# Kernel optimization log

Measured on AMD Instinct MI355X. Metric: run time of the kernel, lower is better.

The kernel has to match this reference:

```python
import math
import jax, jax.numpy as jnp
import numpy as np

B, S, H, M, E = 4, 4096, 1024, 1024, 16
CAPACITY_FACTOR = 2.0
ROUTE_SCALE = 1.0


def setup_inputs() -> dict:
    key = jax.random.key(0)
    ks = jax.random.split(key, 8)
    return {
        "hidden_states": jax.random.normal(ks[0], (B, S, H), dtype=jnp.float32),
        "hidden_states_unmodulated": jax.random.normal(ks[1], (B, S, H), dtype=jnp.float32),
        "timestep": jax.random.normal(ks[2], (B, H), dtype=jnp.float32),
        "gate_w": jax.random.normal(ks[3], (2 * H, E), dtype=jnp.float32) * 0.02,
        "gate_up_proj": jax.random.normal(ks[4], (E, H, 2 * M), dtype=jnp.float32) * 0.02,
        "down_proj": jax.random.normal(ks[5], (E, M, H), dtype=jnp.float32) * 0.02,
        "shared_gate_up_w": jax.random.normal(ks[6], (H, 2 * M), dtype=jnp.float32) * 0.02,
        "shared_down_w": jax.random.normal(ks[7], (M, H), dtype=jnp.float32) * 0.02,
    }


def reference(hidden_states, hidden_states_unmodulated, timestep, gate_w,
              gate_up_proj, down_proj, shared_gate_up_w, shared_down_w):
    b, s, h = hidden_states.shape
    e = gate_up_proj.shape[0]
    capacity = max(1, math.ceil(CAPACITY_FACTOR * s / e))  # static per shapes

    # --- router ---
    t = jnp.broadcast_to(timestep[:, None, :], (b, s, h))
    router_input = jnp.concatenate([t, hidden_states_unmodulated], axis=-1)  # [b,s,2h]
    logits = router_input @ gate_w                                           # [b,s,e]
    scores = jax.nn.sigmoid(logits.astype(jnp.float32)).astype(logits.dtype)
    affinity = jnp.swapaxes(scores, 1, 2)                                    # [b,e,s]

    # --- expert-choice top-k ---
    gating, top_idx = jax.lax.top_k(affinity, capacity)                      # [b,e,cap]
    offsets = (jnp.arange(b) * s)[:, None, None]
    gidx = jnp.swapaxes(offsets + top_idx, 0, 1).reshape(-1)                 # [e*b*cap]
    gflat = jnp.swapaxes(gating, 0, 1).reshape(-1)

    # normalize per-token scores over experts that picked the token
    sums = jnp.zeros(b * s, dtype=gflat.dtype).at[gidx].add(gflat)
    gflat = gflat / (sums[gidx] + 1e-12) * ROUTE_SCALE

    # --- dispatch + grouped SwiGLU experts ---
    x_flat = hidden_states.reshape(b * s, h)
    routed = x_flat[gidx].reshape(e, b * capacity, h)
    gu = jnp.einsum('eth,ehf->etf', routed, gate_up_proj)                    # [e,t,2m]
    g, u = jnp.split(gu, 2, axis=-1)
    expert_out = jnp.einsum('etm,emh->eth', jax.nn.silu(g) * u, down_proj)
    expert_out = expert_out.reshape(e * b * capacity, h)
    expert_out = (expert_out.astype(jnp.float32) *
                  gflat.astype(jnp.float32)[:, None]).astype(hidden_states.dtype)

    # --- shared expert (SwiGLUProj order: hidden * silu(gate)) ---
    hgu = hidden_states @ shared_gate_up_w                                   # [b,s,2m]
    hs_, hg = jnp.split(hgu, 2, axis=-1)
    shared = (hs_ * jax.nn.silu(hg)) @ shared_down_w                         # [b,s,h]

    # --- scatter combine ---
    out = shared.reshape(b * s, h).at[gidx].add(expert_out)
    return out.reshape(b, s, h)
```

## Files before the change

kernel.cpp:

```cpp
#include <hip/hip_runtime.h>
#include <math.h>

#define Bb 4
#define Ss 4096
#define Hh 1024
#define Mm 1024
#define Ee 16
#define CAPk 512

typedef unsigned short u16;
typedef __attribute__((ext_vector_type(8))) short short8;
typedef __attribute__((ext_vector_type(4))) float floatx4;
typedef __attribute__((ext_vector_type(4))) unsigned short ushort4v;

__device__ __forceinline__ float silu_f(float x) {
    return x / (1.0f + expf(-x));
}

__device__ __forceinline__ u16 f2b(float x) {
    union { float f; unsigned u; } v; v.f = x;
    unsigned r = (v.u + 0x7fffu + ((v.u >> 16) & 1u)) >> 16;
    return (u16)r;
}

__device__ __forceinline__ void gl_lds16(const void* g, void* l) {
    __builtin_amdgcn_global_load_lds((const __attribute__((address_space(1))) void*)g,
                                     (__attribute__((address_space(3))) void*)l, 16, 0, 0);
}


__global__ __launch_bounds__(256)
void router_scores(const float* __restrict__ hsu,
                   const float* __restrict__ gate_w,
                   const float* __restrict__ timestep,
                   float* __restrict__ scores) {
    __shared__ float Xs[64 * 64];
    __shared__ float Gs[64 * 16];
    const int t = threadIdx.x;
    const int row0 = blockIdx.x * 64;
    const int b = row0 >> 12;
    const int wave = t >> 6, lane = t & 63;
    const int e0 = wave * 4;
    const float* gw2 = gate_w + (size_t)Hh * Ee;

    float tl0 = 0.f, tl1 = 0.f, tl2 = 0.f, tl3 = 0.f;
    {
        const float* tsrow = timestep + (size_t)b * Hh;
#pragma unroll
        for (int j = 0; j < 16; ++j) {
            int h = lane + 64 * j;
            float tv = tsrow[h];
            const float* gw = gate_w + (size_t)h * Ee + e0;
            tl0 += tv * gw[0]; tl1 += tv * gw[1]; tl2 += tv * gw[2]; tl3 += tv * gw[3];
        }
#pragma unroll
        for (int off = 32; off; off >>= 1) {
            tl0 += __shfl_xor(tl0, off); tl1 += __shfl_xor(tl1, off);
            tl2 += __shfl_xor(tl2, off); tl3 += __shfl_xor(tl3, off);
        }
    }

    float acc0 = 0.f, acc1 = 0.f, acc2 = 0.f, acc3 = 0.f;

    for (int k0 = 0; k0 < Hh; k0 += 64) {
        __syncthreads();
#pragma unroll
        for (int r = 0; r < 4; ++r) {
            int tok = r * 16 + (t >> 4);
            int cslot = t & 15;
            int g = cslot ^ (tok & 15);
            const float* src = hsu + (size_t)(row0 + tok) * Hh + k0 + g * 4;
            char* dst = (char*)Xs + r * 4096 + wave * 1024;
            gl_lds16(src, dst);
        }
        {
            const float* src = gw2 + (size_t)k0 * Ee + t * 4;
            char* dst = (char*)Gs + wave * 1024;
            gl_lds16(src, dst);
        }
        __syncthreads();
#pragma unroll
        for (int kk = 0; kk < 64; kk += 4) {
            int slot = (kk >> 2) ^ (lane & 15);
            float4 a = *(const float4*)&Xs[lane * 64 + slot * 4];
            float4 g0 = *(const float4*)&Gs[(kk + 0) * Ee + e0];
            float4 g1 = *(const float4*)&Gs[(kk + 1) * Ee + e0];
            float4 g2 = *(const float4*)&Gs[(kk + 2) * Ee + e0];
            float4 g3 = *(const float4*)&Gs[(kk + 3) * Ee + e0];
            acc0 += a.x * g0.x; acc0 += a.y * g1.x; acc0 += a.z * g2.x; acc0 += a.w * g3.x;
            acc1 += a.x * g0.y; acc1 += a.y * g1.y; acc1 += a.z * g2.y; acc1 += a.w * g3.y;
            acc2 += a.x * g0.z; acc2 += a.y * g1.z; acc2 += a.z * g2.z; acc2 += a.w * g3.z;
            acc3 += a.x * g0.w; acc3 += a.y * g1.w; acc3 += a.z * g2.w; acc3 += a.w * g3.w;
        }
    }
    const int s = (row0 + lane) & (Ss - 1);
    float l0 = acc0 + tl0;
    float l1 = acc1 + tl1;
    float l2 = acc2 + tl2;
    float l3 = acc3 + tl3;
    scores[((size_t)(b * Ee + e0 + 0)) * Ss + s] = 1.f / (1.f + expf(-l0));
    scores[((size_t)(b * Ee + e0 + 1)) * Ss + s] = 1.f / (1.f + expf(-l1));
    scores[((size_t)(b * Ee + e0 + 2)) * Ss + s] = 1.f / (1.f + expf(-l2));
    scores[((size_t)(b * Ee + e0 + 3)) * Ss + s] = 1.f / (1.f + expf(-l3));
}

__global__ __launch_bounds__(1024)
void topk_kernel(const float* __restrict__ scores,
                 int* __restrict__ sel_idx,
                 float* __restrict__ sel_gate,
                 float* __restrict__ sums,
                 int* __restrict__ cnt) {
    const int be = blockIdx.x;
    const float* sc = scores + (size_t)be * Ss;
    const int t = threadIdx.x;
    const int lane = t & 63, w = t >> 6;
    __shared__ unsigned hist[256];
    __shared__ unsigned wtot[16];
    __shared__ unsigned sh_prefix;
    __shared__ int sh_need;
    __shared__ unsigned cnt_gt;

    if (t < 256) { sums[be * 256 + t] = 0.f; cnt[be * 256 + t] = 0; }

    unsigned vu[4];
#pragma unroll
    for (int i = 0; i < 4; ++i) vu[i] = __float_as_uint(sc[t * 4 + i]);

    unsigned prefix = 0;
    int need = CAPk;
    for (int pass = 0; pass < 4; ++pass) {
        const int shift = 24 - 8 * pass;
        if (t < 256) hist[t] = 0;
        __syncthreads();
#pragma unroll
        for (int i = 0; i < 4; ++i) {
            unsigned u = vu[i];
            bool ok = (pass == 0) || ((u >> (shift + 8)) == prefix);
            if (ok) atomicAdd(&hist[(u >> shift) & 255u], 1u);
        }
        __syncthreads();
        unsigned hval = (t < 256) ? hist[t] : 0u;
        unsigned s = hval;
#pragma unroll
        for (int d = 1; d < 64; d <<= 1) {
            unsigned o = __shfl_down(s, d);
            if (lane + d < 64) s += o;
        }
        if (lane == 0 && w < 4) wtot[w] = s;
        __syncthreads();
        if (t < 256) {
#pragma unroll
            for (int w2 = 0; w2 < 4; ++w2)
                if (w2 > w) s += wtot[w2];
            unsigned Snext = s - hval;
            if (s >= (unsigned)need && Snext < (unsigned)need) {
                sh_prefix = (prefix << 8) | (unsigned)t;
                sh_need = need - (int)Snext;
            }
        }
        __syncthreads();
        prefix = sh_prefix;
        need = sh_need;
        __syncthreads();
    }
    const unsigned T = prefix;
    const int need_eq = need;
    const unsigned ngt = (unsigned)(CAPk - need_eq);

    int myeq = 0;
#pragma unroll
    for (int i = 0; i < 4; ++i) myeq += (vu[i] == T) ? 1 : 0;
    unsigned e = (unsigned)myeq;
#pragma unroll
    for (int d = 1; d < 64; d <<= 1) {
        unsigned o = __shfl_up(e, d);
        if (lane >= d) e += o;
    }
    if (lane == 63) wtot[w] = e;
    if (t == 0) cnt_gt = 0;
    __syncthreads();
    unsigned eqr = e - (unsigned)myeq;
#pragma unroll
    for (int w2 = 0; w2 < 16; ++w2)
        if (w2 < w) eqr += wtot[w2];
#pragma unroll
    for (int i = 0; i < 4; ++i) {
        unsigned u = vu[i];
        int s = t * 4 + i;
        if (u > T) {
            unsigned slot = atomicAdd(&cnt_gt, 1u);
            sel_idx[(size_t)be * CAPk + slot] = s;
            sel_gate[(size_t)be * CAPk + slot] = __uint_as_float(u);
        } else if (u == T) {
            if ((int)eqr < need_eq) {
                unsigned slot = ngt + eqr;
                sel_idx[(size_t)be * CAPk + slot] = s;
                sel_gate[(size_t)be * CAPk + slot] = __uint_as_float(u);
            }
            eqr++;
        }
    }
}

__global__ void accum_kernel(const int* __restrict__ sel_idx,
                             const float* __restrict__ sel_gate,
                             float* __restrict__ sums) {
    int g = blockIdx.x * 256 + threadIdx.x;
    int be = g / CAPk;
    int b = be >> 4;
    atomicAdd(&sums[b * Ss + sel_idx[g]], sel_gate[g]);
}

__global__ void finalize_kernel(const int* __restrict__ sel_idx,
                                const float* __restrict__ sel_gate,
                                const float* __restrict__ sums,
                                int* __restrict__ slot_token,
                                float* __restrict__ slot_w,
                                int* __restrict__ cnt,
                                int* __restrict__ inv) {
    int g = blockIdx.x * 256 + threadIdx.x;
    int be = g / CAPk, c = g % CAPk;
    int b = be >> 4, e = be & 15;
    int token = b * Ss + sel_idx[g];
    float wv = sel_gate[g] / (sums[token] + 1e-12f);
    int o = (e * Bb + b) * CAPk + c;
    slot_token[o] = token;
    slot_w[o] = wv;
    int pos = atomicAdd(&cnt[token], 1);
    inv[(size_t)token * 16 + pos] = o;
}

__global__ __launch_bounds__(256)
void combine_kernel(const int* __restrict__ cnt, const int* __restrict__ inv,
                    const float* __restrict__ eo, float* __restrict__ out) {
    const int token = blockIdx.x;
    const int k = cnt[token];
    if (k == 0) return;
    const int col = threadIdx.x * 4;
    const size_t rowoff = (size_t)token * 1024 + col;
    float4 acc = *(const float4*)(out + rowoff);
    for (int j = 0; j < k; ++j) {
        int slot = inv[token * 16 + j];
        float4 v = *(const float4*)(eo + (size_t)slot * 1024 + col);
        acc.x += v.x; acc.y += v.y; acc.z += v.z; acc.w += v.w;
    }
    *(float4*)(out + rowoff) = acc;
}


__global__ __launch_bounds__(256)
void convert_bf16(const float* __restrict__ src, u16* __restrict__ dst) {
    int i = (blockIdx.x * 256 + threadIdx.x) * 4;
    float4 v = *(const float4*)(src + i);
    ushort4v o = { f2b(v.x), f2b(v.y), f2b(v.z), f2b(v.w) };
    *(ushort4v*)(dst + i) = o;
}

__global__ __launch_bounds__(256)
void transpose_bf16(const float* __restrict__ W, u16* __restrict__ Wt,
                    int N, size_t zsrc, size_t zdst) {
    __shared__ float tile[64][65];
    int n0 = blockIdx.x * 64, k0 = blockIdx.y * 64, z = blockIdx.z;
    const float* Ws = W + (size_t)z * zsrc;
    u16* Wd = Wt + (size_t)z * zdst;
    int t = threadIdx.x;
    int lr = t >> 4, lc = (t & 15) * 4;
#pragma unroll
    for (int i = 0; i < 4; ++i) {
        float4 v = *(const float4*)&Ws[(size_t)(k0 + lr + i * 16) * N + n0 + lc];
        tile[lr + i * 16][lc + 0] = v.x;
        tile[lr + i * 16][lc + 1] = v.y;
        tile[lr + i * 16][lc + 2] = v.z;
        tile[lr + i * 16][lc + 3] = v.w;
    }
    __syncthreads();
    int on = t >> 2;
    int ok0 = (t & 3) * 16;
    u16 buf[16];
#pragma unroll
    for (int j = 0; j < 16; ++j) buf[j] = f2b(tile[ok0 + j][on]);
    u16* dp = &Wd[(size_t)(n0 + on) * 1024 + k0 + ok0];
    *(short8*)(dp) = *(short8*)&buf[0];
    *(short8*)(dp + 8) = *(short8*)&buf[8];
}


__device__ __forceinline__ void stage_tile512(const u16* __restrict__ grow, int k0,
                                              u16* lds, int t) {
#pragma unroll
    for (int r = 0; r < 2; ++r) {
        int ci = r * 512 + t;
        int m = ci >> 3;
        int c = (ci & 7) ^ (m & 7);
        const u16* src = grow + (size_t)m * 1024 + k0 + c * 8;
        u16* dst = lds + ((r * 8192 + (t >> 6) * 1024) >> 1);
        gl_lds16(src, dst);
    }
}

__device__ __forceinline__ void stage_rows512(const u16* __restrict__ A, const int* rid,
                                              int k0, u16* lds, int t) {
#pragma unroll
    for (int r = 0; r < 2; ++r) {
        int ci = r * 512 + t;
        int m = ci >> 3;
        int c = (ci & 7) ^ (m & 7);
        const u16* src = A + (size_t)rid[r] * 1024 + k0 + c * 8;
        u16* dst = lds + ((r * 8192 + (t >> 6) * 1024) >> 1);
        gl_lds16(src, dst);
    }
}

template <bool SILU_FIRST, bool GATHER>
__global__ __launch_bounds__(512, 4)
void gemm1_mfma(const u16* __restrict__ A, int a_row0, int zstride,
                const u16* __restrict__ W1t, u16* __restrict__ act,
                const int* __restrict__ slot_token, int e_base) {
    __shared__ u16 lA[128 * 64];
    __shared__ u16 lB1[128 * 64];
    __shared__ u16 lB2[128 * 64];
    const int t = threadIdx.x;
    const int n0 = blockIdx.x * 128;
    const int bm0 = blockIdx.y * 128;
    const int z = blockIdx.z;
    const int zb = z * zstride;
    const u16* B1row = W1t + ((size_t)z * 2048 + n0) * 1024;
    const u16* B2row = B1row + (size_t)1024 * 1024;
    const int lane = t & 63;
    const int wv = t >> 6;
    const int wm = wv & 1, wn = wv >> 1;
    const int quad = lane >> 4, l15 = lane & 15;

    int rid[2];
#pragma unroll
    for (int r = 0; r < 2; ++r) {
        int m = (t >> 3) + 64 * r;
        rid[r] = GATHER ? slot_token[(e_base + z) * (Bb * CAPk) + bm0 + m]
                        : (a_row0 + zb + bm0 + m);
    }

    floatx4 zero4 = {0.f, 0.f, 0.f, 0.f};
    floatx4 acc1[4][2], acc2[4][2];
#pragma unroll
    for (int i = 0; i < 4; ++i)
#pragma unroll
        for (int j = 0; j < 2; ++j) { acc1[i][j] = zero4; acc2[i][j] = zero4; }

    for (int k0 = 0; k0 < 1024; k0 += 64) {
        __syncthreads();
        stage_rows512(A, rid, k0, lA, t);
        stage_tile512(B1row, k0, lB1, t);
        stage_tile512(B2row, k0, lB2, t);
        __syncthreads();
#pragma unroll
        for (int kc = 0; kc < 2; ++kc) {
            short8 af[4], bf1[2], bf2[2];
#pragma unroll
            for (int mi = 0; mi < 4; ++mi) {
                int m = wm * 64 + mi * 16 + l15;
                int off = m * 64 + (((kc * 4 + quad) ^ (m & 7)) * 8);
                af[mi] = *(const short8*)&lA[off];
            }
#pragma unroll
            for (int ni = 0; ni < 2; ++ni) {
                int n = wn * 32 + ni * 16 + l15;
                int off = n * 64 + (((kc * 4 + quad) ^ (n & 7)) * 8);
                bf1[ni] = *(const short8*)&lB1[off];
                bf2[ni] = *(const short8*)&lB2[off];
            }
#pragma unroll
            for (int mi = 0; mi < 4; ++mi)
#pragma unroll
                for (int ni = 0; ni < 2; ++ni) {
                    acc1[mi][ni] = __builtin_amdgcn_mfma_f32_16x16x32_bf16(af[mi], bf1[ni], acc1[mi][ni], 0, 0, 0);
                    acc2[mi][ni] = __builtin_amdgcn_mfma_f32_16x16x32_bf16(af[mi], bf2[ni], acc2[mi][ni], 0, 0, 0);
                }
        }
    }
#pragma unroll
    for (int mi = 0; mi < 4; ++mi)
#pragma unroll
        for (int ni = 0; ni < 2; ++ni)
#pragma unroll
            for (int r = 0; r < 4; ++r) {
                int m = wm * 64 + mi * 16 + quad * 4 + r;
                int n = wn * 32 + ni * 16 + l15;
                float c1 = acc1[mi][ni][r], c2 = acc2[mi][ni][r];
                float v = SILU_FIRST ? silu_f(c1) * c2 : c1 * silu_f(c2);
                act[(size_t)(zb + bm0 + m) * 1024 + n0 + n] = f2b(v);
            }
}

template <int MODE>
__global__ __launch_bounds__(512, 4)
void gemm2_mfma(const u16* __restrict__ A, int zstride,
                const u16* __restrict__ W2t,
                const int* __restrict__ slot_token, const float* __restrict__ slot_w,
                float* __restrict__ out, int out_row0, int e_base) {
    __shared__ u16 lA[128 * 64];
    __shared__ u16 lB[128 * 64];
    __shared__ int s_tok[(MODE == 1) ? 128 : 1];
    __shared__ float s_w[(MODE == 1 || MODE == 2) ? 128 : 1];
    const int t = threadIdx.x;
    const int n0 = blockIdx.x * 128;
    const int bm0 = blockIdx.y * 128;
    const int z = blockIdx.z;
    const int zb = z * zstride;
    const u16* Arow = A + (size_t)(zb + bm0) * 1024;
    const u16* Brow = W2t + ((size_t)z * 1024 + n0) * 1024;
    const int lane = t & 63;
    const int wv = t >> 6;
    const int wm = wv & 1, wn = wv >> 1;
    const int quad = lane >> 4, l15 = lane & 15;

    if ((MODE == 1 || MODE == 2) && t < 128) {
        int gi = (e_base + z) * (Bb * CAPk) + bm0 + t;
        if (MODE == 1) s_tok[t] = slot_token[gi];
        s_w[t] = slot_w[gi];
    }

    floatx4 zero4 = {0.f, 0.f, 0.f, 0.f};
    floatx4 acc[4][2];
#pragma unroll
    for (int i = 0; i < 4; ++i)
#pragma unroll
        for (int j = 0; j < 2; ++j) acc[i][j] = zero4;

    for (int k0 = 0; k0 < 1024; k0 += 64) {
        __syncthreads();
        stage_tile512(Arow, k0, lA, t);
        stage_tile512(Brow, k0, lB, t);
        __syncthreads();
#pragma unroll
        for (int kc = 0; kc < 2; ++kc) {
            short8 af[4], bf[2];
#pragma unroll
            for (int mi = 0; mi < 4; ++mi) {
                int m = wm * 64 + mi * 16 + l15;
                int off = m * 64 + (((kc * 4 + quad) ^ (m & 7)) * 8);
                af[mi] = *(const short8*)&lA[off];
            }
#pragma unroll
            for (int ni = 0; ni < 2; ++ni) {
                int n = wn * 32 + ni * 16 + l15;
                int off = n * 64 + (((kc * 4 + quad) ^ (n & 7)) * 8);
                bf[ni] = *(const short8*)&lB[off];
            }
#pragma unroll
            for (int mi = 0; mi < 4; ++mi)
#pragma unroll
                for (int ni = 0; ni < 2; ++ni)
                    acc[mi][ni] = __builtin_amdgcn_mfma_f32_16x16x32_bf16(af[mi], bf[ni], acc[mi][ni], 0, 0, 0);
        }
    }
#pragma unroll
    for (int mi = 0; mi < 4; ++mi)
#pragma unroll
        for (int ni = 0; ni < 2; ++ni)
#pragma unroll
            for (int r = 0; r < 4; ++r) {
                int m = wm * 64 + mi * 16 + quad * 4 + r;
                int n = wn * 32 + ni * 16 + l15;
                float c = acc[mi][ni][r];
                if (MODE == 1) {
                    atomicAdd(&out[(size_t)s_tok[m] * 1024 + n0 + n], c * s_w[m]);
                } else if (MODE == 2) {
                    out[((size_t)((e_base + z) * (Bb * CAPk) + bm0 + m)) * 1024 + n0 + n] = c * s_w[m];
                } else {
                    out[(size_t)(out_row0 + bm0 + m) * 1024 + n0 + n] = c;
                }
            }
}


extern "C" void kernel_launch(void* const* d_in, const int* in_sizes, int n_in,
                              void* d_out, int out_size, void* d_ws, size_t ws_size,
                              hipStream_t stream) {
    const float* hidden   = (const float*)d_in[0];
    const float* hsu      = (const float*)d_in[1];
    const float* timestep = (const float*)d_in[2];
    const float* gate_w   = (const float*)d_in[3];
    const float* gate_up  = (const float*)d_in[4];
    const float* down     = (const float*)d_in[5];
    const float* sh_gu    = (const float*)d_in[6];
    const float* sh_dn    = (const float*)d_in[7];
    float* out = (float*)d_out;

    char* p = (char*)d_ws;
    auto alloc = [&](size_t bytes) { char* r = p; p += (bytes + 255) & ~(size_t)255; return r; };
    float* scores    = (float*)alloc((size_t)Bb * Ee * Ss * 4);
    int*   sel_idx   = (int*)  alloc((size_t)Bb * Ee * CAPk * 4);
    float* sel_gate  = (float*)alloc((size_t)Bb * Ee * CAPk * 4);
    float* sums      = (float*)alloc((size_t)Bb * Ss * 4);
    int*   slot_token= (int*)  alloc((size_t)Ee * Bb * CAPk * 4);
    float* slot_w    = (float*)alloc((size_t)Ee * Bb * CAPk * 4);
    int*   cnt       = (int*)  alloc((size_t)Bb * Ss * 4);
    int*   inv       = (int*)  alloc((size_t)Bb * Ss * 16 * 4);
    u16*   Xb        = (u16*)  alloc((size_t)16384 * 1024 * 2);
    char* phase = p;
    long long avail = (long long)((char*)d_ws + ws_size - phase);
    if (avail < 0) avail = 0;

    const long long eo_bytes     = (long long)32768 * 1024 * 4;
    const long long per_e        = ((long long)2048 * 1024 + 1024 * 1024 +
                                    (long long)2048 * 1024) * 2;
    const long long shared_fixed = ((long long)2048 * 1024 + 1024 * 1024) * 2;

    convert_bf16<<<16384, 256, 0, stream>>>(hidden, Xb);
    router_scores<<<(Bb * Ss) / 64, 256, 0, stream>>>(hsu, gate_w, timestep, scores);
    topk_kernel<<<Bb * Ee, 1024, 0, stream>>>(scores, sel_idx, sel_gate, sums, cnt);
    accum_kernel<<<(Bb * Ee * CAPk) / 256, 256, 0, stream>>>(sel_idx, sel_gate, sums);
    finalize_kernel<<<(Bb * Ee * CAPk) / 256, 256, 0, stream>>>(sel_idx, sel_gate, sums,
                                                                slot_token, slot_w, cnt, inv);

    long long min_shared = shared_fixed + (long long)128 * 2048;
    bool use_eo = (avail >= eo_bytes + (per_e > min_shared ? per_e : min_shared));

    if (use_eo) {
        float* eo = (float*)phase;
        char* ph2 = phase + eo_bytes;
        long long avail2 = avail - eo_bytes;

        {
            int g = (int)(avail2 / per_e);
            if (g < 1) g = 1;
            if (g > Ee) g = Ee;
            u16* Wt1r = (u16*)ph2;
            u16* Wt2r = Wt1r + (size_t)g * 2048 * 1024;
            u16* actR = Wt2r + (size_t)g * 1024 * 1024;

            for (int e0 = 0; e0 < Ee; e0 += g) {
                int cg = Ee - e0; if (cg > g) cg = g;
                transpose_bf16<<<dim3(32, 16, cg), 256, 0, stream>>>(
                    gate_up + (size_t)e0 * 2097152, Wt1r, 2048, 2097152, 2097152);
                transpose_bf16<<<dim3(16, 16, cg), 256, 0, stream>>>(
                    down + (size_t)e0 * 1048576, Wt2r, 1024, 1048576, 1048576);
                gemm1_mfma<true, true><<<dim3(8, 16, cg), 512, 0, stream>>>(
                    Xb, 0, 2048, Wt1r, actR, slot_token, e0);
                gemm2_mfma<2><<<dim3(8, 16, cg), 512, 0, stream>>>(
                    actR, 2048, Wt2r, slot_token, slot_w, eo, 0, e0);
            }
        }

        {
            u16* Wt1s = (u16*)ph2;
            u16* Wt2s = Wt1s + (size_t)2048 * 1024;
            u16* actS = Wt2s + (size_t)1024 * 1024;
            long long room = (avail2 - shared_fixed) / 2048;
            room &= ~127LL;
            int R = (int)(room > 16384 ? 16384 : room);
            if (R < 128) R = 128;

            transpose_bf16<<<dim3(32, 16, 1), 256, 0, stream>>>(sh_gu, Wt1s, 2048, 0, 0);
            transpose_bf16<<<dim3(16, 16, 1), 256, 0, stream>>>(sh_dn, Wt2s, 1024, 0, 0);
            for (int r0 = 0; r0 < Bb * Ss; r0 += R) {
                int cur = Bb * Ss - r0; if (cur > R) cur = R;
                gemm1_mfma<false, false><<<dim3(8, cur / 128, 1), 512, 0, stream>>>(
                    Xb, r0, 0, Wt1s, actS, nullptr, 0);
                gemm2_mfma<0><<<dim3(8, cur / 128, 1), 512, 0, stream>>>(
                    actS, 0, Wt2s, nullptr, nullptr, out, r0, 0);
            }
        }

        combine_kernel<<<Bb * Ss, 256, 0, stream>>>(cnt, inv, eo, out);
    } else {
        {
            u16* Wt1s = (u16*)phase;
            u16* Wt2s = Wt1s + (size_t)2048 * 1024;
            u16* actS = Wt2s + (size_t)1024 * 1024;
            long long room = (avail - shared_fixed) / 2048;
            room &= ~127LL;
            int R = (int)(room > 16384 ? 16384 : room);
            if (R < 128) R = 128;

            transpose_bf16<<<dim3(32, 16, 1), 256, 0, stream>>>(sh_gu, Wt1s, 2048, 0, 0);
            transpose_bf16<<<dim3(16, 16, 1), 256, 0, stream>>>(sh_dn, Wt2s, 1024, 0, 0);
            for (int r0 = 0; r0 < Bb * Ss; r0 += R) {
                int cur = Bb * Ss - r0; if (cur > R) cur = R;
                gemm1_mfma<false, false><<<dim3(8, cur / 128, 1), 512, 0, stream>>>(
                    Xb, r0, 0, Wt1s, actS, nullptr, 0);
                gemm2_mfma<0><<<dim3(8, cur / 128, 1), 512, 0, stream>>>(
                    actS, 0, Wt2s, nullptr, nullptr, out, r0, 0);
            }
        }
        {
            int g = (int)(avail / per_e);
            if (g < 1) g = 1;
            if (g > Ee) g = Ee;
            u16* Wt1r = (u16*)phase;
            u16* Wt2r = Wt1r + (size_t)g * 2048 * 1024;
            u16* actR = Wt2r + (size_t)g * 1024 * 1024;

            for (int e0 = 0; e0 < Ee; e0 += g) {
                int cg = Ee - e0; if (cg > g) cg = g;
                transpose_bf16<<<dim3(32, 16, cg), 256, 0, stream>>>(
                    gate_up + (size_t)e0 * 2097152, Wt1r, 2048, 2097152, 2097152);
                transpose_bf16<<<dim3(16, 16, cg), 256, 0, stream>>>(
                    down + (size_t)e0 * 1048576, Wt2r, 1024, 1048576, 1048576);
                gemm1_mfma<true, true><<<dim3(8, 16, cg), 512, 0, stream>>>(
                    Xb, 0, 2048, Wt1r, actR, slot_token, e0);
                gemm2_mfma<1><<<dim3(8, 16, cg), 512, 0, stream>>>(
                    actR, 2048, Wt2r, slot_token, slot_w, out, 0, e0);
            }
        }
    }
}
```

Baseline: 821.2 us.

## Fuse launches: merged convert+router, rank-based routing, single-pass transposes and GEMMs

Merges the bf16 conversion of hidden states into the router kernel and replaces the accum/finalize atomic routing kernels with a per-token rank map built by topk and consumed by one route_build kernel. Adds a fast path that, when workspace allows, transposes all expert and shared weights in one launch and runs each expert GEMM once over all 16 experts instead of in groups. This cuts kernel launches, atomics and tail effects between small kernels, at the cost of a larger workspace footprint and an extra rank array the size of the scores.

```diff
diff --git a/kernel.cpp b/kernel.cpp
--- a/kernel.cpp
+++ b/kernel.cpp
@@ -30,14 +30,23 @@
 
 
 __global__ __launch_bounds__(256)
-void router_scores(const float* __restrict__ hsu,
-                   const float* __restrict__ gate_w,
-                   const float* __restrict__ timestep,
-                   float* __restrict__ scores) {
+void conv_router(const float* __restrict__ hidden, u16* __restrict__ Xb,
+                 const float* __restrict__ hsu,
+                 const float* __restrict__ gate_w,
+                 const float* __restrict__ timestep,
+                 float* __restrict__ scores) {
+    const int t = threadIdx.x;
+    if (blockIdx.x < 16384) {
+        int i = (blockIdx.x * 256 + t) * 4;
+        float4 v = *(const float4*)(hidden + i);
+        ushort4v o = { f2b(v.x), f2b(v.y), f2b(v.z), f2b(v.w) };
+        *(ushort4v*)(Xb + i) = o;
+        return;
+    }
     __shared__ float Xs[64 * 64];
     __shared__ float Gs[64 * 16];
-    const int t = threadIdx.x;
-    const int row0 = blockIdx.x * 64;
+    const int rbid = blockIdx.x - 16384;
+    const int row0 = rbid * 64;
     const int b = row0 >> 12;
     const int wave = t >> 6, lane = t & 63;
     const int e0 = wave * 4;
@@ -106,12 +115,10 @@
 
 __global__ __launch_bounds__(1024)
 void topk_kernel(const float* __restrict__ scores,
-                 int* __restrict__ sel_idx,
-                 float* __restrict__ sel_gate,
-                 float* __restrict__ sums,
-                 int* __restrict__ cnt) {
+                 int* __restrict__ rank) {
     const int be = blockIdx.x;
     const float* sc = scores + (size_t)be * Ss;
+    int* rk = rank + (size_t)be * Ss;
     const int t = threadIdx.x;
     const int lane = t & 63, w = t >> 6;
     __shared__ unsigned hist[256];
@@ -120,7 +127,8 @@
     __shared__ int sh_need;
     __shared__ unsigned cnt_gt;
 
-    if (t < 256) { sums[be * 256 + t] = 0.f; cnt[be * 256 + t] = 0; }
+#pragma unroll
+    for (int i = 0; i < 4; ++i) rk[t * 4 + i] = -1;
 
     unsigned vu[4];
 #pragma unroll
@@ -189,45 +197,47 @@
         int s = t * 4 + i;
         if (u > T) {
             unsigned slot = atomicAdd(&cnt_gt, 1u);
-            sel_idx[(size_t)be * CAPk + slot] = s;
-            sel_gate[(size_t)be * CAPk + slot] = __uint_as_float(u);
+            rk[s] = (int)slot;
         } else if (u == T) {
             if ((int)eqr < need_eq) {
-                unsigned slot = ngt + eqr;
-                sel_idx[(size_t)be * CAPk + slot] = s;
-                sel_gate[(size_t)be * CAPk + slot] = __uint_as_float(u);
+                rk[s] = (int)(ngt + eqr);
             }
             eqr++;
         }
     }
 }
 
-__global__ void accum_kernel(const int* __restrict__ sel_idx,
-                             const float* __restrict__ sel_gate,
-                             float* __restrict__ sums) {
-    int g = blockIdx.x * 256 + threadIdx.x;
-    int be = g / CAPk;
-    int b = be >> 4;
-    atomicAdd(&sums[b * Ss + sel_idx[g]], sel_gate[g]);
-}
-
-__global__ void finalize_kernel(const int* __restrict__ sel_idx,
-                                const float* __restrict__ sel_gate,
-                                const float* __restrict__ sums,
-                                int* __restrict__ slot_token,
-                                float* __restrict__ slot_w,
-                                int* __restrict__ cnt,
-                                int* __restrict__ inv) {
-    int g = blockIdx.x * 256 + threadIdx.x;
-    int be = g / CAPk, c = g % CAPk;
-    int b = be >> 4, e = be & 15;
-    int token = b * Ss + sel_idx[g];
-    float wv = sel_gate[g] / (sums[token] + 1e-12f);
-    int o = (e * Bb + b) * CAPk + c;
-    slot_token[o] = token;
-    slot_w[o] = wv;
-    int pos = atomicAdd(&cnt[token], 1);
-    inv[(size_t)token * 16 + pos] = o;
+__global__ __launch_bounds__(256)
+void route_build(const float* __restrict__ scores, const int* __restrict__ rank,
+                 int* __restrict__ slot_token, float* __restrict__ slot_w,
+                 int* __restrict__ cnt, int* __restrict__ inv) {
+    const int token = blockIdx.x * 256 + threadIdx.x;
+    const int b = token >> 12, s = token & (Ss - 1);
+    int rr[16];
+    float gg[16];
+    float sum = 0.f;
+#pragma unroll
+    for (int e = 0; e < 16; ++e) {
+        size_t idx = (size_t)(b * Ee + e) * Ss + s;
+        int r = rank[idx];
+        rr[e] = r;
+        float g = (r >= 0) ? scores[idx] : 0.f;
+        gg[e] = g;
+        sum += g;
+    }
+    int pos = 0;
+#pragma unroll
+    for (int e = 0; e < 16; ++e) {
+        if (rr[e] >= 0) {
+            float wv = gg[e] / (sum + 1e-12f);
+            int o = (e * Bb + b) * CAPk + rr[e];
+            slot_token[o] = token;
+            slot_w[o] = wv;
+            inv[token * 16 + pos] = o;
+            ++pos;
+        }
+    }
+    cnt[token] = pos;
 }
 
 __global__ __launch_bounds__(256)
@@ -248,22 +258,8 @@
 }
 
 
-__global__ __launch_bounds__(256)
-void convert_bf16(const float* __restrict__ src, u16* __restrict__ dst) {
-    int i = (blockIdx.x * 256 + threadIdx.x) * 4;
-    float4 v = *(const float4*)(src + i);
-    ushort4v o = { f2b(v.x), f2b(v.y), f2b(v.z), f2b(v.w) };
-    *(ushort4v*)(dst + i) = o;
-}
-
-__global__ __launch_bounds__(256)
-void transpose_bf16(const float* __restrict__ W, u16* __restrict__ Wt,
-                    int N, size_t zsrc, size_t zdst) {
-    __shared__ float tile[64][65];
-    int n0 = blockIdx.x * 64, k0 = blockIdx.y * 64, z = blockIdx.z;
-    const float* Ws = W + (size_t)z * zsrc;
-    u16* Wd = Wt + (size_t)z * zdst;
-    int t = threadIdx.x;
+__device__ __forceinline__ void tpose_body(const float* __restrict__ Ws, u16* __restrict__ Wd,
+                                           int N, int n0, int k0, float tile[64][65], int t) {
     int lr = t >> 4, lc = (t & 15) * 4;
 #pragma unroll
     for (int i = 0; i < 4; ++i) {
@@ -282,6 +278,42 @@
     u16* dp = &Wd[(size_t)(n0 + on) * 1024 + k0 + ok0];
     *(short8*)(dp) = *(short8*)&buf[0];
     *(short8*)(dp + 8) = *(short8*)&buf[8];
+}
+
+__global__ __launch_bounds__(256)
+void transpose_bf16(const float* __restrict__ W, u16* __restrict__ Wt,
+                    int N, size_t zsrc, size_t zdst) {
+    __shared__ float tile[64][65];
+    int n0 = blockIdx.x * 64, k0 = blockIdx.y * 64, z = blockIdx.z;
+    tpose_body(W + (size_t)z * zsrc, Wt + (size_t)z * zdst, N, n0, k0, tile, threadIdx.x);
+}
+
+__global__ __launch_bounds__(256)
+void transpose_all(const float* __restrict__ gate_up, const float* __restrict__ down,
+                   const float* __restrict__ sh_gu, const float* __restrict__ sh_dn,
+                   u16* __restrict__ Wt1r, u16* __restrict__ Wt2r,
+                   u16* __restrict__ Wt1s, u16* __restrict__ Wt2s) {
+    __shared__ float tile[64][65];
+    const int id = blockIdx.x;
+    const float* Ws; u16* Wd; int N, n0, k0;
+    if (id < 8192) {
+        int z = id >> 9, r = id & 511;
+        n0 = (r & 31) * 64; k0 = (r >> 5) * 64; N = 2048;
+        Ws = gate_up + (size_t)z * 2097152; Wd = Wt1r + (size_t)z * 2097152;
+    } else if (id < 12288) {
+        int i2 = id - 8192; int z = i2 >> 8, r = i2 & 255;
+        n0 = (r & 15) * 64; k0 = (r >> 4) * 64; N = 1024;
+        Ws = down + (size_t)z * 1048576; Wd = Wt2r + (size_t)z * 1048576;
+    } else if (id < 12800) {
+        int r = id - 12288;
+        n0 = (r & 31) * 64; k0 = (r >> 5) * 64; N = 2048;
+        Ws = sh_gu; Wd = Wt1s;
+    } else {
+        int r = id - 12800;
+        n0 = (r & 15) * 64; k0 = (r >> 4) * 64; N = 1024;
+        Ws = sh_dn; Wd = Wt2s;
+    }
+    tpose_body(Ws, Wd, N, n0, k0, tile, threadIdx.x);
 }
 
 
@@ -489,9 +521,7 @@
     char* p = (char*)d_ws;
     auto alloc = [&](size_t bytes) { char* r = p; p += (bytes + 255) & ~(size_t)255; return r; };
     float* scores    = (float*)alloc((size_t)Bb * Ee * Ss * 4);
-    int*   sel_idx   = (int*)  alloc((size_t)Bb * Ee * CAPk * 4);
-    float* sel_gate  = (float*)alloc((size_t)Bb * Ee * CAPk * 4);
-    float* sums      = (float*)alloc((size_t)Bb * Ss * 4);
+    int*   rank      = (int*)  alloc((size_t)Bb * Ee * Ss * 4);
     int*   slot_token= (int*)  alloc((size_t)Ee * Bb * CAPk * 4);
     float* slot_w    = (float*)alloc((size_t)Ee * Bb * CAPk * 4);
     int*   cnt       = (int*)  alloc((size_t)Bb * Ss * 4);
@@ -505,22 +535,47 @@
     const long long per_e        = ((long long)2048 * 1024 + 1024 * 1024 +
                                     (long long)2048 * 1024) * 2;
     const long long shared_fixed = ((long long)2048 * 1024 + 1024 * 1024) * 2;
-
-    convert_bf16<<<16384, 256, 0, stream>>>(hidden, Xb);
-    router_scores<<<(Bb * Ss) / 64, 256, 0, stream>>>(hsu, gate_w, timestep, scores);
-    topk_kernel<<<Bb * Ee, 1024, 0, stream>>>(scores, sel_idx, sel_gate, sums, cnt);
-    accum_kernel<<<(Bb * Ee * CAPk) / 256, 256, 0, stream>>>(sel_idx, sel_gate, sums);
-    finalize_kernel<<<(Bb * Ee * CAPk) / 256, 256, 0, stream>>>(sel_idx, sel_gate, sums,
-                                                                slot_token, slot_w, cnt, inv);
-
-    long long min_shared = shared_fixed + (long long)128 * 2048;
-    bool use_eo = (avail >= eo_bytes + (per_e > min_shared ? per_e : min_shared));
-
-    if (use_eo) {
+    const long long fast_need    = ((long long)16 * 2048 * 1024 +
+                                    (long long)16 * 1024 * 1024 +
+                                    (long long)16 * 2048 * 1024 +
+                                    (long long)2048 * 1024 +
+                                    (long long)1024 * 1024) * 2;
+
+    conv_router<<<16384 + (Bb * Ss) / 64, 256, 0, stream>>>(hidden, Xb, hsu, gate_w,
+                                                            timestep, scores);
+    topk_kernel<<<Bb * Ee, 1024, 0, stream>>>(scores, rank);
+    route_build<<<(Bb * Ss) / 256, 256, 0, stream>>>(scores, rank, slot_token, slot_w,
+                                                     cnt, inv);
+
+    bool use_eo = (avail >= eo_bytes + (per_e > (shared_fixed + (long long)128 * 2048)
+                                        ? per_e : (shared_fixed + (long long)128 * 2048)));
+    bool fast   = use_eo && (avail - eo_bytes >= fast_need);
+
+    if (fast) {
+        float* eo = (float*)phase;
+        char* ph2 = phase + eo_bytes;
+        u16* Wt1r = (u16*)ph2;
+        u16* Wt2r = Wt1r + (size_t)16 * 2048 * 1024;
+        u16* actR = Wt2r + (size_t)16 * 1024 * 1024;
+        u16* Wt1s = actR + (size_t)16 * 2048 * 1024;
+        u16* Wt2s = Wt1s + (size_t)2048 * 1024;
+        u16* actS = Wt1r;
+
+        transpose_all<<<13056, 256, 0, stream>>>(gate_up, down, sh_gu, sh_dn,
+                                                 Wt1r, Wt2r, Wt1s, Wt2s);
+        gemm1_mfma<true, true><<<dim3(8, 16, 16), 512, 0, stream>>>(
+            Xb, 0, 2048, Wt1r, actR, slot_token, 0);
+        gemm2_mfma<2><<<dim3(8, 16, 16), 512, 0, stream>>>(
+            actR, 2048, Wt2r, slot_token, slot_w, eo, 0, 0);
+        gemm1_mfma<false, false><<<dim3(8, 128, 1), 512, 0, stream>>>(
+            Xb, 0, 0, Wt1s, actS, nullptr, 0);
+        gemm2_mfma<0><<<dim3(8, 128, 1), 512, 0, stream>>>(
+            actS, 0, Wt2s, nullptr, nullptr, out, 0, 0);
+        combine_kernel<<<Bb * Ss, 256, 0, stream>>>(cnt, inv, eo, out);
+    } else if (use_eo) {
         float* eo = (float*)phase;
         char* ph2 = phase + eo_bytes;
         long long avail2 = avail - eo_bytes;
-
         {
             int g = (int)(avail2 / per_e);
             if (g < 1) g = 1;
@@ -528,7 +583,6 @@
             u16* Wt1r = (u16*)ph2;
             u16* Wt2r = Wt1r + (size_t)g * 2048 * 1024;
             u16* actR = Wt2r + (size_t)g * 1024 * 1024;
-
             for (int e0 = 0; e0 < Ee; e0 += g) {
                 int cg = Ee - e0; if (cg > g) cg = g;
                 transpose_bf16<<<dim3(32, 16, cg), 256, 0, stream>>>(
@@ -541,7 +595,6 @@
                     actR, 2048, Wt2r, slot_token, slot_w, eo, 0, e0);
             }
         }
-
         {
             u16* Wt1s = (u16*)ph2;
             u16* Wt2s = Wt1s + (size_t)2048 * 1024;
@@ -550,7 +603,6 @@
             room &= ~127LL;
             int R = (int)(room > 16384 ? 16384 : room);
             if (R < 128) R = 128;
-
             transpose_bf16<<<dim3(32, 16, 1), 256, 0, stream>>>(sh_gu, Wt1s, 2048, 0, 0);
             transpose_bf16<<<dim3(16, 16, 1), 256, 0, stream>>>(sh_dn, Wt2s, 1024, 0, 0);
             for (int r0 = 0; r0 < Bb * Ss; r0 += R) {
@@ -561,7 +613,6 @@
                     actS, 0, Wt2s, nullptr, nullptr, out, r0, 0);
             }
         }
-
         combine_kernel<<<Bb * Ss, 256, 0, stream>>>(cnt, inv, eo, out);
     } else {
         {
@@ -572,7 +623,6 @@
             room &= ~127LL;
             int R = (int)(room > 16384 ? 16384 : room);
             if (R < 128) R = 128;
-
             transpose_bf16<<<dim3(32, 16, 1), 256, 0, stream>>>(sh_gu, Wt1s, 2048, 0, 0);
             transpose_bf16<<<dim3(16, 16, 1), 256, 0, stream>>>(sh_dn, Wt2s, 1024, 0, 0);
             for (int r0 = 0; r0 < Bb * Ss; r0 += R) {
@@ -590,7 +640,6 @@
             u16* Wt1r = (u16*)phase;
             u16* Wt2r = Wt1r + (size_t)g * 2048 * 1024;
             u16* actR = Wt2r + (size_t)g * 1024 * 1024;
-
             for (int e0 = 0; e0 < Ee; e0 += g) {
                 int cg = Ee - e0; if (cg > g) cg = g;
                 transpose_bf16<<<dim3(32, 16, cg), 256, 0, stream>>>(
```

New measurement: 834.1 us. Within noise of the previous version (+1.6%).
